# Kernel optimization log

Hardware: AMD Instinct MI355X
Metric: run time of the kernel (lower is better)

Reference implementation:

```python
import jax, jax.numpy as jnp
import numpy as np

D_MODEL = 256
EXPAND = 2
MAX_STEPS = 6
DILATIONS = (1, 2, 4)
EPS = 1e-6


def setup_inputs() -> dict:
    key = jax.random.key(0)
    ks = jax.random.split(key, 12)
    B, C, H, W = 8, D_MODEL, 64, 64
    d, dh = D_MODEL, D_MODEL * EXPAND
    init_logit = float(np.log(0.1 / (0.25 - 0.1 + 1e-08)))
    s = 1.0 / np.sqrt(d)
    return {
        "u": jax.random.normal(ks[0], (B, C, H, W), jnp.float32),
        "forcing": jax.random.normal(ks[1], (B, C, H, W), jnp.float32),
        "diff_logits": jnp.full((3, d), init_logit, jnp.float32),
        "w1": jax.random.uniform(ks[2], (d, dh), jnp.float32, -s, s),
        "b1": jax.random.uniform(ks[3], (dh,), jnp.float32, -s, s),
        "w2": jax.random.uniform(ks[4], (dh, d), jnp.float32, -1.0 / np.sqrt(dh), 1.0 / np.sqrt(dh)),
        "b2": jax.random.uniform(ks[5], (d,), jnp.float32, -1.0 / np.sqrt(dh), 1.0 / np.sqrt(dh)),
        "wf": jax.random.uniform(ks[6], (d, d), jnp.float32, -s, s),
        "bf": jax.random.uniform(ks[7], (d,), jnp.float32, -s, s),
        "wi": jax.random.uniform(ks[8], (d, d), jnp.float32, -s, s),
        "bi": jax.random.uniform(ks[9], (d,), jnp.float32, -s, s),
        "wc": jax.random.uniform(ks[10], (d, d), jnp.float32, -s, s),
        "bc": jax.random.uniform(ks[11], (d,), jnp.float32, -s, s),
        "norm_scale": jnp.ones((d,), jnp.float32),
        "log_dt": jnp.asarray(np.log(0.1), jnp.float32),
        "alpha_mem": jnp.asarray(0.1, jnp.float32),
        "alpha_force": jnp.asarray(0.1, jnp.float32),
    }


def _laplacian(u, diff_logits):
    # multi-dilation 5-point reflect-padded stencil, per-channel coeffs
    out = jnp.zeros_like(u)
    for i, d in enumerate(DILATIONS):
        coeff = 0.25 * jax.nn.sigmoid(diff_logits[i])  # (C,)
        p = jnp.pad(u, ((0, 0), (0, 0), (d, d), (d, d)), mode="reflect")
        lap = (p[:, :, d:-d, 2 * d:] + p[:, :, d:-d, :-2 * d]
               + p[:, :, 2 * d:, d:-d] + p[:, :, :-2 * d, d:-d] - 4.0 * u)
        out = out + coeff[None, :, None, None] * lap
    return out


def reference(u, forcing, diff_logits, w1, b1, w2, b2, wf, bf, wi, bi, wc, bc,
              norm_scale, log_dt, alpha_mem, alpha_force):
    B, C, H, W = u.shape
    dt = jnp.clip(jnp.exp(log_dt), 0.01, 0.3)
    h = jnp.zeros((B, C), u.dtype)
    inv_sqrt_c = 1.0 / float(np.sqrt(C))
    for t in range(MAX_STEPS):
        diff = _laplacian(u, diff_logits)
        # per-cell reaction MLP on channel axis (exact GELU, matching torch)
        hdn = jax.nn.gelu(jnp.einsum("bchw,ce->behw", u, w1) + b1[None, :, None, None],
                          approximate=False)
        react = jnp.einsum("behw,ec->bchw", hdn, w2) + b2[None, :, None, None]
        # gated global memory on pooled features
        pooled = u.mean(axis=(2, 3))  # (B, C)
        f = jax.nn.sigmoid(pooled @ wf + bf)
        i_ = jax.nn.sigmoid(pooled @ wi + bi)
        c = jnp.tanh(pooled @ wc + bc)
        h = h * f + i_ * c
        du = diff + react + alpha_mem * h[:, :, None, None] + alpha_force * forcing
        u = u + dt * du
        if (t + 1) % 2 == 0:
            # RMSNorm over channel dim
            rms = jnp.sqrt(jnp.sum(u * u, axis=1, keepdims=True)) * inv_sqrt_c
            u = u / (rms + EPS) * norm_scale[None, :, None, None]
    return u
```

## Files before the change

### kernel.cpp

```cpp
#include <hip/hip_runtime.h>
#include <math.h>

constexpr int NB = 8, NC = 256, NE = 512, NH = 64, NW = 64, NHW = NH * NW;
constexpr int STEPS = 6;

typedef short bfrag8 __attribute__((ext_vector_type(8)));
typedef float f32x4 __attribute__((ext_vector_type(4)));

__device__ __forceinline__ float sigm_(float x) { return 1.f / (1.f + expf(-x)); }
__device__ __forceinline__ float gelu_(float x) {
    const float t2 = fmaf(0.0713548162f * x, x * x, 1.5957691216f * x);
    return x / (1.f + __expf(-t2));
}
__device__ __forceinline__ ushort f2bf(float f) {
    unsigned u = __builtin_bit_cast(unsigned, f);
    unsigned r = (u + 0x7fffu + ((u >> 16) & 1u)) >> 16;
    return (ushort)r;
}
__device__ __forceinline__ float bf2f(ushort us) {
    return __builtin_bit_cast(float, (unsigned)us << 16);
}
__device__ __forceinline__ void gload16(const void* g, void* l) {
    __builtin_amdgcn_global_load_lds((const __attribute__((address_space(1))) void*)g,
                                     (__attribute__((address_space(3))) void*)l, 16, 0, 0);
}

__global__ void wt_kernel(const float* __restrict__ w1, const float* __restrict__ w2,
                          const float* __restrict__ dlog,
                          const float* __restrict__ wf, const float* __restrict__ wi,
                          const float* __restrict__ wc,
                          ushort* __restrict__ w1t, ushort* __restrict__ w2t,
                          float* __restrict__ dcoef, ushort* __restrict__ wgb) {
    const int bid = blockIdx.x, tid = threadIdx.x;
    if (bid < NE) {
        w1t[bid * NC + tid] = f2bf(w1[(size_t)tid * NE + bid]);
    } else if (bid < NE + NC) {
        const int c = bid - NE;
        for (int e = tid; e < NE; e += 256)
            w2t[c * NE + e] = f2bf(w2[(size_t)e * NC + c]);
    } else if (bid == NE + NC) {
#pragma unroll
        for (int i = 0; i < 3; ++i)
            dcoef[i * NC + tid] = 0.25f * sigm_(dlog[i * NC + tid]);
    } else {
        const int k = bid - (NE + NC + 1);
        wgb[(0 * NC + k) * NC + tid] = f2bf(wf[(size_t)k * NC + tid]);
        wgb[(1 * NC + k) * NC + tid] = f2bf(wi[(size_t)k * NC + tid]);
        wgb[(2 * NC + k) * NC + tid] = f2bf(wc[(size_t)k * NC + tid]);
    }
}

__global__ void fconv_kernel(const float* __restrict__ fin, ushort* __restrict__ fout) {
    const size_t i8 = ((size_t)blockIdx.x * 256 + threadIdx.x) * 8;
    const float4 a = *reinterpret_cast<const float4*>(fin + i8);
    const float4 b = *reinterpret_cast<const float4*>(fin + i8 + 4);
    uint4 o;
    o.x = (unsigned)f2bf(a.x) | ((unsigned)f2bf(a.y) << 16);
    o.y = (unsigned)f2bf(a.z) | ((unsigned)f2bf(a.w) << 16);
    o.z = (unsigned)f2bf(b.x) | ((unsigned)f2bf(b.y) << 16);
    o.w = (unsigned)f2bf(b.z) | ((unsigned)f2bf(b.w) << 16);
    *reinterpret_cast<uint4*>(fout + i8) = o;
}

__global__ __launch_bounds__(256) void rs0_kernel(const float* __restrict__ u,
                                                  float* __restrict__ rowsums) {
    const int b = blockIdx.x >> 6, y = blockIdx.x & 63;
    const int c = threadIdx.x;
    const float* rp = u + ((size_t)b * NC + c) * NHW + (size_t)y * NW;
    float s = 0.f;
#pragma unroll
    for (int i = 0; i < 16; ++i) {
        const float4 v = *reinterpret_cast<const float4*>(rp + i * 4);
        s += (v.x + v.y) + (v.z + v.w);
    }
    rowsums[((size_t)b * 64 + y) * NC + c] = s;
}

__global__ __launch_bounds__(768) void gates_kernel(
    const float* __restrict__ rowsums, const ushort* __restrict__ wgb,
    const float* __restrict__ bfv, const float* __restrict__ biv,
    const float* __restrict__ bcv,
    float* __restrict__ h, const int first) {
    const int b = blockIdx.x;
    const int tid = threadIdx.x;
    const int g = tid >> 8, c = tid & 255;
    __shared__ float sp[256];
    __shared__ float psum[3][256];
    __shared__ float gf[256], gi[256];
    const int y0 = (g == 0) ? 0 : (g == 1) ? 21 : 42;
    const int y1 = (g == 0) ? 21 : (g == 1) ? 42 : 64;
    const float* rs = rowsums + (size_t)b * 64 * NC + c;
    float s = 0.f;
    for (int y = y0; y < y1; ++y) s += rs[y * NC];
    psum[g][c] = s;
    __syncthreads();
    if (g == 0) sp[c] = (psum[0][c] + psum[1][c] + psum[2][c]) * (1.f / 4096.f);
    __syncthreads();
    const ushort* W16 = wgb + (size_t)g * NC * NC;
    const float* Bv = (g == 0) ? bfv : (g == 1) ? biv : bcv;
    float aA = 0.f, aB = 0.f, aC = 0.f, aD = 0.f;
#pragma unroll 4
    for (int k = 0; k < 256; k += 4) {
        aA = fmaf(sp[k],     bf2f(W16[(k)     * NC + c]), aA);
        aB = fmaf(sp[k + 1], bf2f(W16[(k + 1) * NC + c]), aB);
        aC = fmaf(sp[k + 2], bf2f(W16[(k + 2) * NC + c]), aC);
        aD = fmaf(sp[k + 3], bf2f(W16[(k + 3) * NC + c]), aD);
    }
    const float a = ((aA + aB) + (aC + aD)) + Bv[c];
    if (g == 0) gf[c] = sigm_(a);
    else if (g == 1) gi[c] = sigm_(a);
    __syncthreads();
    if (g == 2) {
        const float cc = tanhf(a);
        const float hold = first ? 0.f : h[b * NC + c];
        h[b * NC + c] = hold * gf[c] + gi[c] * cc;
    }
}

__global__ __launch_bounds__(512, 4) void step_kernel(
    const ushort* __restrict__ w1t, const ushort* __restrict__ w2t,
    const float* __restrict__ b1, const float* __restrict__ b2,
    const float* __restrict__ uin, const ushort* __restrict__ forc,
    const float* __restrict__ dcoef, const float* __restrict__ hbuf,
    const float* __restrict__ nsc, const float* __restrict__ p_logdt,
    const float* __restrict__ p_am, const float* __restrict__ p_af,
    const int do_norm, float* __restrict__ uout, float* __restrict__ rowsums) {
    __shared__ __align__(16) char pool[75776];
    ushort* Xs  = (ushort*)pool;
    ushort* WAu = (ushort*)(pool + 32768);
    ushort* WBu = (ushort*)(pool + 49152);
    ushort* Hsu = (ushort*)(pool + 65536);

    const int tid = threadIdx.x;
    const int wv = tid >> 6, lane = tid & 63;
    const int r16 = lane & 15, kg = lane >> 4;
    const int work = (blockIdx.x & 7) * 64 + (blockIdx.x >> 3);
    const int b = work >> 6, y = work & 63;

    const float* ub = uin + (size_t)b * NC * NHW;
    const float* uyb = ub + (size_t)y * NW;

#pragma unroll
    for (int i = 0; i < 2; ++i) {
        const int idx = i * 512 + tid, row = idx >> 5, s = idx & 31;
        gload16(w1t + (size_t)row * NC + ((s ^ (row & 7)) << 3), WAu + idx * 8);
    }
#pragma unroll
    for (int tt = 0; tt < 2; ++tt) {
        const int id = tt * 512 + tid;
        const int pg_ = id & 15, cg_ = id >> 4;
        const int px0 = pg_ * 4, c0 = cg_ * 4;
        const float4 r0 = *(const float4*)(uyb + (size_t)(c0 + 0) * NHW + px0);
        const float4 r1 = *(const float4*)(uyb + (size_t)(c0 + 1) * NHW + px0);
        const float4 r2 = *(const float4*)(uyb + (size_t)(c0 + 2) * NHW + px0);
        const float4 r3 = *(const float4*)(uyb + (size_t)(c0 + 3) * NHW + px0);
        const int slot = c0 >> 3, sub = c0 & 7;
        const float a0[4] = {r0.x, r0.y, r0.z, r0.w};
        const float a1[4] = {r1.x, r1.y, r1.z, r1.w};
        const float a2[4] = {r2.x, r2.y, r2.z, r2.w};
        const float a3[4] = {r3.x, r3.y, r3.z, r3.w};
#pragma unroll
        for (int i2 = 0; i2 < 4; ++i2) {
            const int px = px0 + i2;
            ushort4 xv;
            xv.x = f2bf(a0[i2]);
            xv.y = f2bf(a1[i2]);
            xv.z = f2bf(a2[i2]);
            xv.w = f2bf(a3[i2]);
            *(ushort4*)(Xs + px * 256 + ((slot ^ (px & 7)) << 3) + sub) = xv;
        }
    }

    f32x4 acc2[2][4];
#pragma unroll
    for (int ct = 0; ct < 2; ++ct)
#pragma unroll
        for (int p = 0; p < 4; ++p) acc2[ct][p] = (f32x4){0.f, 0.f, 0.f, 0.f};

    const int eh = wv >> 2, pq = wv & 3;
    __syncthreads();

    bfrag8 xf[8];
    {
        const int rB = pq * 16 + r16;
#pragma unroll
        for (int kk = 0; kk < 8; ++kk) {
            const int g = kk * 4 + kg;
            xf[kk] = *(const bfrag8*)(Xs + rB * 256 + ((g ^ (rB & 7)) << 3));
        }
    }

    for (int ec = 0; ec < 16; ++ec) {
#pragma unroll
        for (int i = 0; i < 2; ++i) {
            const int idx = i * 512 + tid, row = idx >> 2, s = idx & 3;
            const int sc = (s ^ ((row >> 1) & 3)) << 3;
            gload16(w2t + (size_t)row * NE + ec * 32 + sc, WBu + idx * 8);
        }
        f32x4 acc1 = (f32x4){0.f, 0.f, 0.f, 0.f};
        const int rA = eh * 16 + r16;
#pragma unroll
        for (int kk = 0; kk < 8; ++kk) {
            const int g = kk * 4 + kg;
            const bfrag8 a = *(const bfrag8*)(WAu + rA * 256 + ((g ^ (rA & 7)) << 3));
            acc1 = __builtin_amdgcn_mfma_f32_16x16x32_bf16(a, xf[kk], acc1, 0, 0, 0);
        }
        ushort* Hc = Hsu + (ec & 1) * 2560;
        {
            const int el = eh * 16 + kg * 4;
            const float4 b1v = *(const float4*)(b1 + ec * 32 + el);
            ushort4 hv;
            hv.x = f2bf(gelu_(acc1[0] + b1v.x));
            hv.y = f2bf(gelu_(acc1[1] + b1v.y));
            hv.z = f2bf(gelu_(acc1[2] + b1v.z));
            hv.w = f2bf(gelu_(acc1[3] + b1v.w));
            *(ushort4*)(Hc + (pq * 16 + r16) * 40 + el) = hv;
        }
        __syncthreads();
        if (ec < 15) {
#pragma unroll
            for (int i = 0; i < 2; ++i) {
                const int idx = i * 512 + tid, row = idx >> 5, s = idx & 31;
                gload16(w1t + (size_t)((ec + 1) * 32 + row) * NC + ((s ^ (row & 7)) << 3),
                        WAu + idx * 8);
            }
        }
#pragma unroll
        for (int ct = 0; ct < 2; ++ct) {
            const int rowA = wv * 32 + ct * 16 + r16;
            const bfrag8 a2 = *(const bfrag8*)(WBu + rowA * 32 + ((kg ^ ((rowA >> 1) & 3)) << 3));
#pragma unroll
            for (int p = 0; p < 4; ++p) {
                const bfrag8 bf2 = *(const bfrag8*)(Hc + (p * 16 + r16) * 40 + kg * 8);
                acc2[ct][p] = __builtin_amdgcn_mfma_f32_16x16x32_bf16(a2, bf2, acc2[ct][p], 0, 0, 0);
            }
        }
        __syncthreads();
    }

    float* trh = (float*)pool;
    float* su  = (float*)(pool + 35328);
    const int eg2 = tid >> 4, pg = tid & 15, x0p = pg * 4;
    const float dt = fminf(fmaxf(expf(p_logdt[0]), 0.01f), 0.3f);
    const float am = p_am[0], afc = p_af[0];
    const ushort* frow = forc + (size_t)b * NC * NHW + (size_t)y * NW;

    float unew[2][4][4];

#pragma unroll
    for (int h2 = 0; h2 < 2; ++h2) {
        __syncthreads();
        if ((wv >> 2) == h2) {
#pragma unroll
            for (int ct = 0; ct < 2; ++ct)
#pragma unroll
                for (int p = 0; p < 4; ++p)
#pragma unroll
                    for (int j = 0; j < 4; ++j)
                        trh[((wv & 3) * 32 + ct * 16 + kg * 4 + j) * 69 + p * 16 + r16] =
                            acc2[ct][p][j];
        }
#pragma unroll
        for (int i = 0; i < 4; ++i) {
            const int idx = i * 512 + tid;
            const int r = idx >> 4, q = (idx & 15) * 4;
            *(float4*)&su[r * 69 + q] =
                *(const float4*)(ub + (size_t)(h2 * 128 + r) * NHW + (size_t)y * NW + q);
        }
        __syncthreads();
#pragma unroll
        for (int jc = 0; jc < 4; ++jc) {
            const int crel = eg2 * 4 + jc;
            const int c = h2 * 128 + crel;
            const float co0 = dcoef[c];
            const float co1 = dcoef[NC + c];
            const float co2 = dcoef[2 * NC + c];
            const float hterm = am * hbuf[b * NC + c];
            const float b2v = b2[c];
            const float* up = ub + (size_t)c * NHW;

            float ym[6][4];
            const int dy[6] = {-1, 1, -2, 2, -4, 4};
#pragma unroll
            for (int n = 0; n < 6; ++n) {
                int ry = y + dy[n];
                ry = ry < 0 ? -ry : (ry > 63 ? 126 - ry : ry);
                const float4 t = *reinterpret_cast<const float4*>(up + (size_t)ry * NW + x0p);
                ym[n][0] = t.x; ym[n][1] = t.y; ym[n][2] = t.z; ym[n][3] = t.w;
            }
            const uint2 fr = *reinterpret_cast<const uint2*>(frow + (size_t)c * NHW + x0p);
            float fv[4];
            fv[0] = bf2f((ushort)(fr.x & 0xffff));
            fv[1] = bf2f((ushort)(fr.x >> 16));
            fv[2] = bf2f((ushort)(fr.y & 0xffff));
            fv[3] = bf2f((ushort)(fr.y >> 16));
            const f32x4 rv = *reinterpret_cast<const f32x4*>(&trh[crel * 69 + x0p]);
#pragma unroll
            for (int ip = 0; ip < 4; ++ip) {
                const int x = x0p + ip;
                const float uc = su[crel * 69 + x];
                int xm, xp2;
                float dsum = 0.f, lap;
                xm = x - 1; xm = xm < 0 ? -xm : xm;
                xp2 = x + 1; xp2 = xp2 > 63 ? 126 - xp2 : xp2;
                lap = su[crel * 69 + xm] + su[crel * 69 + xp2] + ym[0][ip] + ym[1][ip] - 4.f * uc;
                dsum = fmaf(co0, lap, dsum);
                xm = x - 2; xm = xm < 0 ? -xm : xm;
                xp2 = x + 2; xp2 = xp2 > 63 ? 126 - xp2 : xp2;
                lap = su[crel * 69 + xm] + su[crel * 69 + xp2] + ym[2][ip] + ym[3][ip] - 4.f * uc;
                dsum = fmaf(co1, lap, dsum);
                xm = x - 4; xm = xm < 0 ? -xm : xm;
                xp2 = x + 4; xp2 = xp2 > 63 ? 126 - xp2 : xp2;
                lap = su[crel * 69 + xm] + su[crel * 69 + xp2] + ym[4][ip] + ym[5][ip] - 4.f * uc;
                dsum = fmaf(co2, lap, dsum);

                const float du_ = dsum + rv[ip] + b2v + hterm + afc * fv[ip];
                unew[h2][jc][ip] = uc + dt * du_;
            }
        }
    }
    __syncthreads();

    float* redc   = (float*)(pool + 35328);
    float* inv64p = (float*)(pool + 70656);
    if (do_norm) {
        float ps[4] = {0.f, 0.f, 0.f, 0.f};
#pragma unroll
        for (int h2 = 0; h2 < 2; ++h2)
#pragma unroll
            for (int jc = 0; jc < 4; ++jc)
#pragma unroll
                for (int ip = 0; ip < 4; ++ip)
                    ps[ip] = fmaf(unew[h2][jc][ip], unew[h2][jc][ip], ps[ip]);
        *reinterpret_cast<f32x4*>(&redc[eg2 * 69 + x0p]) = (f32x4){ps[0], ps[1], ps[2], ps[3]};
        __syncthreads();
        if (tid < 64) {
            float s = 0.f;
#pragma unroll
            for (int g = 0; g < 32; ++g) s += redc[g * 69 + tid];
            inv64p[tid] = 1.f / (sqrtf(s) * 0.0625f + 1e-6f);
        }
    }
    __syncthreads();

    float* sums = (float*)(pool + 35328);
    float persum[2][4];
    float* uob = uout + (size_t)b * NC * NHW + (size_t)y * NW;
#pragma unroll
    for (int h2 = 0; h2 < 2; ++h2) {
#pragma unroll
        for (int jc = 0; jc < 4; ++jc) {
            const int c = h2 * 128 + eg2 * 4 + jc;
            const float ns = do_norm ? nsc[c] : 1.f;
            float vv[4];
#pragma unroll
            for (int ip = 0; ip < 4; ++ip) {
                float v = unew[h2][jc][ip];
                if (do_norm) v *= inv64p[x0p + ip] * ns;
                vv[ip] = v;
            }
            persum[h2][jc] = (vv[0] + vv[1]) + (vv[2] + vv[3]);
            float4 o; o.x = vv[0]; o.y = vv[1]; o.z = vv[2]; o.w = vv[3];
            *reinterpret_cast<float4*>(uob + (size_t)c * NHW + x0p) = o;
            sums[c * 17 + pg] = persum[h2][jc];
        }
    }
    __syncthreads();
    if (tid < 256) {
        float s = 0.f;
#pragma unroll
        for (int g = 0; g < 16; ++g) s += sums[tid * 17 + g];
        rowsums[((size_t)b * 64 + y) * NC + tid] = s;
    }
}

extern "C" void kernel_launch(void* const* d_in, const int* in_sizes, int n_in,
                              void* d_out, int out_size, void* d_ws, size_t ws_size,
                              hipStream_t stream) {
    (void)in_sizes; (void)n_in; (void)out_size; (void)ws_size;
    const float* u0      = (const float*)d_in[0];
    const float* forcing = (const float*)d_in[1];
    const float* dlog    = (const float*)d_in[2];
    const float* w1      = (const float*)d_in[3];
    const float* b1      = (const float*)d_in[4];
    const float* w2      = (const float*)d_in[5];
    const float* b2      = (const float*)d_in[6];
    const float* wf      = (const float*)d_in[7];
    const float* bfv     = (const float*)d_in[8];
    const float* wi      = (const float*)d_in[9];
    const float* biv     = (const float*)d_in[10];
    const float* wc      = (const float*)d_in[11];
    const float* bcv     = (const float*)d_in[12];
    const float* nsc     = (const float*)d_in[13];
    const float* p_logdt = (const float*)d_in[14];
    const float* p_am    = (const float*)d_in[15];
    const float* p_af    = (const float*)d_in[16];

    float* uout = (float*)d_out;

    char* w = (char*)d_ws;
    float*  uA     = (float*)w;   w += (size_t)NB * NC * NHW * 4;
    ushort* forc   = (ushort*)w;  w += (size_t)NB * NC * NHW * 2;
    ushort* w1t    = (ushort*)w;  w += (size_t)NE * NC * 2;
    ushort* w2t    = (ushort*)w;  w += (size_t)NC * NE * 2;
    ushort* wgb    = (ushort*)w;  w += (size_t)3 * NC * NC * 2;
    float* rowsums = (float*)w;   w += (size_t)NB * NH * NC * 4;
    float* hbuf    = (float*)w;   w += (size_t)NB * NC * 4;
    float* dcoef   = (float*)w;   w += (size_t)3 * NC * 4;

    wt_kernel<<<NE + NC + 1 + NC, 256, 0, stream>>>(w1, w2, dlog, wf, wi, wc,
                                                    w1t, w2t, dcoef, wgb);
    fconv_kernel<<<4096, 256, 0, stream>>>(forcing, forc);
    rs0_kernel<<<NB * NH, 256, 0, stream>>>(u0, rowsums);

    const float* src = u0;
    for (int t = 0; t < STEPS; ++t) {
        float* dst = (t & 1) ? uout : uA;
        gates_kernel<<<NB, 768, 0, stream>>>(rowsums, wgb, bfv, biv, bcv, hbuf, t == 0);
        step_kernel<<<NB * NH, 512, 0, stream>>>(w1t, w2t, b1, b2, src, forc, dcoef,
                                                 hbuf, nsc, p_logdt, p_am, p_af,
                                                 ((t + 1) % 2) == 0, dst, rowsums);
        src = dst;
    }
}
```

Measured before the change: 575.1 us.

## Fuse gated memory computation into step kernel and pad stencil rows

Removes the separate gates kernel launch per step: every step block redundantly reduces the pooled row sums, computes the f/i/c gates from transposed bf16 weights, and updates h, with row sums and h ping-ponged between buffers to avoid races. The horizontal stencil now reads from a reflect-padded shared row using vector loads instead of per-element index clamping. This trades six small serial launches for redundant gate GEMV work in all 512 blocks plus extra shared memory and syncs, which may lower occupancy.

```diff
diff --git a/kernel.cpp b/kernel.cpp
--- a/kernel.cpp
+++ b/kernel.cpp
@@ -30,7 +30,7 @@
                           const float* __restrict__ wf, const float* __restrict__ wi,
                           const float* __restrict__ wc,
                           ushort* __restrict__ w1t, ushort* __restrict__ w2t,
-                          float* __restrict__ dcoef, ushort* __restrict__ wgb) {
+                          float* __restrict__ dcoef, ushort* __restrict__ wgt) {
     const int bid = blockIdx.x, tid = threadIdx.x;
     if (bid < NE) {
         w1t[bid * NC + tid] = f2bf(w1[(size_t)tid * NE + bid]);
@@ -43,10 +43,10 @@
         for (int i = 0; i < 3; ++i)
             dcoef[i * NC + tid] = 0.25f * sigm_(dlog[i * NC + tid]);
     } else {
-        const int k = bid - (NE + NC + 1);
-        wgb[(0 * NC + k) * NC + tid] = f2bf(wf[(size_t)k * NC + tid]);
-        wgb[(1 * NC + k) * NC + tid] = f2bf(wi[(size_t)k * NC + tid]);
-        wgb[(2 * NC + k) * NC + tid] = f2bf(wc[(size_t)k * NC + tid]);
+        const int j = bid - (NE + NC + 1);
+        const int g = j >> 8, c = j & 255, k = tid;
+        const float* src = (g == 0) ? wf : (g == 1) ? wi : wc;
+        wgt[(((size_t)g * NC + c) << 8) + k] = f2bf(src[(size_t)k * NC + c]);
     }
 }
 
@@ -76,60 +76,26 @@
     rowsums[((size_t)b * 64 + y) * NC + c] = s;
 }
 
-__global__ __launch_bounds__(768) void gates_kernel(
-    const float* __restrict__ rowsums, const ushort* __restrict__ wgb,
-    const float* __restrict__ bfv, const float* __restrict__ biv,
-    const float* __restrict__ bcv,
-    float* __restrict__ h, const int first) {
-    const int b = blockIdx.x;
-    const int tid = threadIdx.x;
-    const int g = tid >> 8, c = tid & 255;
-    __shared__ float sp[256];
-    __shared__ float psum[3][256];
-    __shared__ float gf[256], gi[256];
-    const int y0 = (g == 0) ? 0 : (g == 1) ? 21 : 42;
-    const int y1 = (g == 0) ? 21 : (g == 1) ? 42 : 64;
-    const float* rs = rowsums + (size_t)b * 64 * NC + c;
-    float s = 0.f;
-    for (int y = y0; y < y1; ++y) s += rs[y * NC];
-    psum[g][c] = s;
-    __syncthreads();
-    if (g == 0) sp[c] = (psum[0][c] + psum[1][c] + psum[2][c]) * (1.f / 4096.f);
-    __syncthreads();
-    const ushort* W16 = wgb + (size_t)g * NC * NC;
-    const float* Bv = (g == 0) ? bfv : (g == 1) ? biv : bcv;
-    float aA = 0.f, aB = 0.f, aC = 0.f, aD = 0.f;
-#pragma unroll 4
-    for (int k = 0; k < 256; k += 4) {
-        aA = fmaf(sp[k],     bf2f(W16[(k)     * NC + c]), aA);
-        aB = fmaf(sp[k + 1], bf2f(W16[(k + 1) * NC + c]), aB);
-        aC = fmaf(sp[k + 2], bf2f(W16[(k + 2) * NC + c]), aC);
-        aD = fmaf(sp[k + 3], bf2f(W16[(k + 3) * NC + c]), aD);
-    }
-    const float a = ((aA + aB) + (aC + aD)) + Bv[c];
-    if (g == 0) gf[c] = sigm_(a);
-    else if (g == 1) gi[c] = sigm_(a);
-    __syncthreads();
-    if (g == 2) {
-        const float cc = tanhf(a);
-        const float hold = first ? 0.f : h[b * NC + c];
-        h[b * NC + c] = hold * gf[c] + gi[c] * cc;
-    }
-}
-
 __global__ __launch_bounds__(512, 4) void step_kernel(
     const ushort* __restrict__ w1t, const ushort* __restrict__ w2t,
     const float* __restrict__ b1, const float* __restrict__ b2,
     const float* __restrict__ uin, const ushort* __restrict__ forc,
-    const float* __restrict__ dcoef, const float* __restrict__ hbuf,
-    const float* __restrict__ nsc, const float* __restrict__ p_logdt,
-    const float* __restrict__ p_am, const float* __restrict__ p_af,
-    const int do_norm, float* __restrict__ uout, float* __restrict__ rowsums) {
-    __shared__ __align__(16) char pool[75776];
+    const float* __restrict__ dcoef, const ushort* __restrict__ wgt,
+    const float* __restrict__ bfv, const float* __restrict__ biv,
+    const float* __restrict__ bcv, const float* __restrict__ hprev,
+    float* __restrict__ hnext, const float* __restrict__ rs_in,
+    float* __restrict__ rs_out, const float* __restrict__ nsc,
+    const float* __restrict__ p_logdt, const float* __restrict__ p_am,
+    const float* __restrict__ p_af, const int do_norm, const int first,
+    float* __restrict__ uout) {
+    __shared__ __align__(16) char pool[79872];
     ushort* Xs  = (ushort*)pool;
     ushort* WAu = (ushort*)(pool + 32768);
     ushort* WBu = (ushort*)(pool + 49152);
     ushort* Hsu = (ushort*)(pool + 65536);
+    float* gsp  = (float*)(pool + 75776);
+    float* gex  = (float*)(pool + 76800);
+    float* hseg = (float*)(pool + 77824);
 
     const int tid = threadIdx.x;
     const int wv = tid >> 6, lane = tid & 63;
@@ -137,6 +103,7 @@
     const int work = (blockIdx.x & 7) * 64 + (blockIdx.x >> 3);
     const int b = work >> 6, y = work & 63;
 
+    const float am = p_am[0];
     const float* ub = uin + (size_t)b * NC * NHW;
     const float* uyb = ub + (size_t)y * NW;
 
@@ -170,6 +137,14 @@
             *(ushort4*)(Xs + px * 256 + ((slot ^ (px & 7)) << 3) + sub) = xv;
         }
     }
+    {
+        const int gc = tid & 255, half = tid >> 8;
+        const float* rs = rs_in + ((size_t)b * 64 + half * 32) * NC + gc;
+        float s = 0.f;
+#pragma unroll 8
+        for (int yy = 0; yy < 32; ++yy) s += rs[yy * NC];
+        (half ? gex : gsp)[gc] = s;
+    }
 
     f32x4 acc2[2][4];
 #pragma unroll
@@ -188,6 +163,55 @@
             const int g = kk * 4 + kg;
             xf[kk] = *(const bfrag8*)(Xs + rB * 256 + ((g ^ (rB & 7)) << 3));
         }
+    }
+    if (tid < 256) gsp[tid] = (gsp[tid] + gex[tid]) * (1.f / 4096.f);
+    __syncthreads();
+
+    float gfv = 0.f, ccv = 0.f;
+    {
+        const int gc = tid & 255, g1 = tid >> 8;
+        const ushort* wrow = wgt + (((size_t)g1 * NC + gc) << 8);
+        float a0 = 0.f, a1 = 0.f;
+#pragma unroll 4
+        for (int k8 = 0; k8 < 256; k8 += 8) {
+            const uint4 wv4 = *(const uint4*)(wrow + k8);
+            a0 = fmaf(gsp[k8 + 0], bf2f((ushort)(wv4.x & 0xffff)), a0);
+            a1 = fmaf(gsp[k8 + 1], bf2f((ushort)(wv4.x >> 16)), a1);
+            a0 = fmaf(gsp[k8 + 2], bf2f((ushort)(wv4.y & 0xffff)), a0);
+            a1 = fmaf(gsp[k8 + 3], bf2f((ushort)(wv4.y >> 16)), a1);
+            a0 = fmaf(gsp[k8 + 4], bf2f((ushort)(wv4.z & 0xffff)), a0);
+            a1 = fmaf(gsp[k8 + 5], bf2f((ushort)(wv4.z >> 16)), a1);
+            a0 = fmaf(gsp[k8 + 6], bf2f((ushort)(wv4.w & 0xffff)), a0);
+            a1 = fmaf(gsp[k8 + 7], bf2f((ushort)(wv4.w >> 16)), a1);
+        }
+        const float av = (a0 + a1) + (g1 == 0 ? bfv[gc] : biv[gc]);
+        if (g1 == 0) gfv = sigm_(av);
+        else gex[gc] = sigm_(av);
+        if (tid < 256) {
+            const ushort* wrow2 = wgt + (((size_t)2 * NC + gc) << 8);
+            float c0 = 0.f, c1 = 0.f;
+#pragma unroll 4
+            for (int k8 = 0; k8 < 256; k8 += 8) {
+                const uint4 wv4 = *(const uint4*)(wrow2 + k8);
+                c0 = fmaf(gsp[k8 + 0], bf2f((ushort)(wv4.x & 0xffff)), c0);
+                c1 = fmaf(gsp[k8 + 1], bf2f((ushort)(wv4.x >> 16)), c1);
+                c0 = fmaf(gsp[k8 + 2], bf2f((ushort)(wv4.y & 0xffff)), c0);
+                c1 = fmaf(gsp[k8 + 3], bf2f((ushort)(wv4.y >> 16)), c1);
+                c0 = fmaf(gsp[k8 + 4], bf2f((ushort)(wv4.z & 0xffff)), c0);
+                c1 = fmaf(gsp[k8 + 5], bf2f((ushort)(wv4.z >> 16)), c1);
+                c0 = fmaf(gsp[k8 + 6], bf2f((ushort)(wv4.w & 0xffff)), c0);
+                c1 = fmaf(gsp[k8 + 7], bf2f((ushort)(wv4.w >> 16)), c1);
+            }
+            ccv = tanhf((c0 + c1) + bcv[gc]);
+        }
+    }
+    __syncthreads();
+    if (tid < 256) {
+        const int gc = tid;
+        const float hp = first ? 0.f : hprev[b * NC + gc];
+        const float h = hp * gfv + gex[gc] * ccv;
+        hseg[gc] = am * h;
+        if (y == 0) hnext[b * NC + gc] = h;
     }
 
     for (int ec = 0; ec < 16; ++ec) {
@@ -242,7 +266,7 @@
     float* su  = (float*)(pool + 35328);
     const int eg2 = tid >> 4, pg = tid & 15, x0p = pg * 4;
     const float dt = fminf(fmaxf(expf(p_logdt[0]), 0.01f), 0.3f);
-    const float am = p_am[0], afc = p_af[0];
+    const float afc = p_af[0];
     const ushort* frow = forc + (size_t)b * NC * NHW + (size_t)y * NW;
 
     float unew[2][4][4];
@@ -264,8 +288,15 @@
         for (int i = 0; i < 4; ++i) {
             const int idx = i * 512 + tid;
             const int r = idx >> 4, q = (idx & 15) * 4;
-            *(float4*)&su[r * 69 + q] =
+            *(float4*)&su[r * 72 + 4 + q] =
                 *(const float4*)(ub + (size_t)(h2 * 128 + r) * NHW + (size_t)y * NW + q);
+        }
+        if (tid < 256) {
+            const int r = tid >> 1, side = tid & 1;
+            const float* gp = ub + (size_t)(h2 * 128 + r) * NHW + (size_t)y * NW;
+            float* sr = &su[r * 72];
+            if (side == 0) { sr[0] = gp[4]; sr[1] = gp[3]; sr[2] = gp[2]; sr[3] = gp[1]; }
+            else { sr[68] = gp[62]; sr[69] = gp[61]; sr[70] = gp[60]; sr[71] = gp[59]; }
         }
         __syncthreads();
 #pragma unroll
@@ -275,7 +306,7 @@
             const float co0 = dcoef[c];
             const float co1 = dcoef[NC + c];
             const float co2 = dcoef[2 * NC + c];
-            const float hterm = am * hbuf[b * NC + c];
+            const float hterm = hseg[c];
             const float b2v = b2[c];
             const float* up = ub + (size_t)c * NHW;
 
@@ -295,23 +326,21 @@
             fv[2] = bf2f((ushort)(fr.y & 0xffff));
             fv[3] = bf2f((ushort)(fr.y >> 16));
             const f32x4 rv = *reinterpret_cast<const f32x4*>(&trh[crel * 69 + x0p]);
+            const f32x4 wm = *reinterpret_cast<const f32x4*>(&su[crel * 72 + pg * 4]);
+            const f32x4 wc4 = *reinterpret_cast<const f32x4*>(&su[crel * 72 + 4 + pg * 4]);
+            const f32x4 wp = *reinterpret_cast<const f32x4*>(&su[crel * 72 + 8 + pg * 4]);
+            const float w[12] = {wm[0], wm[1], wm[2], wm[3],
+                                 wc4[0], wc4[1], wc4[2], wc4[3],
+                                 wp[0], wp[1], wp[2], wp[3]};
 #pragma unroll
             for (int ip = 0; ip < 4; ++ip) {
-                const int x = x0p + ip;
-                const float uc = su[crel * 69 + x];
-                int xm, xp2;
-                float dsum = 0.f, lap;
-                xm = x - 1; xm = xm < 0 ? -xm : xm;
-                xp2 = x + 1; xp2 = xp2 > 63 ? 126 - xp2 : xp2;
-                lap = su[crel * 69 + xm] + su[crel * 69 + xp2] + ym[0][ip] + ym[1][ip] - 4.f * uc;
-                dsum = fmaf(co0, lap, dsum);
-                xm = x - 2; xm = xm < 0 ? -xm : xm;
-                xp2 = x + 2; xp2 = xp2 > 63 ? 126 - xp2 : xp2;
-                lap = su[crel * 69 + xm] + su[crel * 69 + xp2] + ym[2][ip] + ym[3][ip] - 4.f * uc;
+                const float uc = w[4 + ip];
+                float dsum;
+                float lap = (w[3 + ip] + w[5 + ip]) + (ym[0][ip] + ym[1][ip]) - 4.f * uc;
+                dsum = co0 * lap;
+                lap = (w[2 + ip] + w[6 + ip]) + (ym[2][ip] + ym[3][ip]) - 4.f * uc;
                 dsum = fmaf(co1, lap, dsum);
-                xm = x - 4; xm = xm < 0 ? -xm : xm;
-                xp2 = x + 4; xp2 = xp2 > 63 ? 126 - xp2 : xp2;
-                lap = su[crel * 69 + xm] + su[crel * 69 + xp2] + ym[4][ip] + ym[5][ip] - 4.f * uc;
+                lap = (w[ip] + w[8 + ip]) + (ym[4][ip] + ym[5][ip]) - 4.f * uc;
                 dsum = fmaf(co2, lap, dsum);
 
                 const float du_ = dsum + rv[ip] + b2v + hterm + afc * fv[ip];
@@ -322,7 +351,7 @@
     __syncthreads();
 
     float* redc   = (float*)(pool + 35328);
-    float* inv64p = (float*)(pool + 70656);
+    float* inv64p = (float*)(pool + 73728);
     if (do_norm) {
         float ps[4] = {0.f, 0.f, 0.f, 0.f};
 #pragma unroll
@@ -344,7 +373,6 @@
     __syncthreads();
 
     float* sums = (float*)(pool + 35328);
-    float persum[2][4];
     float* uob = uout + (size_t)b * NC * NHW + (size_t)y * NW;
 #pragma unroll
     for (int h2 = 0; h2 < 2; ++h2) {
@@ -359,10 +387,9 @@
                 if (do_norm) v *= inv64p[x0p + ip] * ns;
                 vv[ip] = v;
             }
-            persum[h2][jc] = (vv[0] + vv[1]) + (vv[2] + vv[3]);
             float4 o; o.x = vv[0]; o.y = vv[1]; o.z = vv[2]; o.w = vv[3];
             *reinterpret_cast<float4*>(uob + (size_t)c * NHW + x0p) = o;
-            sums[c * 17 + pg] = persum[h2][jc];
+            sums[c * 17 + pg] = (vv[0] + vv[1]) + (vv[2] + vv[3]);
         }
     }
     __syncthreads();
@@ -370,7 +397,7 @@
         float s = 0.f;
 #pragma unroll
         for (int g = 0; g < 16; ++g) s += sums[tid * 17 + g];
-        rowsums[((size_t)b * 64 + y) * NC + tid] = s;
+        rs_out[((size_t)b * 64 + y) * NC + tid] = s;
     }
 }
 
@@ -403,23 +430,31 @@
     ushort* forc   = (ushort*)w;  w += (size_t)NB * NC * NHW * 2;
     ushort* w1t    = (ushort*)w;  w += (size_t)NE * NC * 2;
     ushort* w2t    = (ushort*)w;  w += (size_t)NC * NE * 2;
-    ushort* wgb    = (ushort*)w;  w += (size_t)3 * NC * NC * 2;
-    float* rowsums = (float*)w;   w += (size_t)NB * NH * NC * 4;
-    float* hbuf    = (float*)w;   w += (size_t)NB * NC * 4;
+    ushort* wgt    = (ushort*)w;  w += (size_t)3 * NC * NC * 2;
+    float* rsA     = (float*)w;   w += (size_t)NB * NH * NC * 4;
+    float* rsB     = (float*)w;   w += (size_t)NB * NH * NC * 4;
+    float* hA      = (float*)w;   w += (size_t)NB * NC * 4;
+    float* hB      = (float*)w;   w += (size_t)NB * NC * 4;
     float* dcoef   = (float*)w;   w += (size_t)3 * NC * 4;
 
-    wt_kernel<<<NE + NC + 1 + NC, 256, 0, stream>>>(w1, w2, dlog, wf, wi, wc,
-                                                    w1t, w2t, dcoef, wgb);
+    wt_kernel<<<NE + NC + 1 + 3 * NC, 256, 0, stream>>>(w1, w2, dlog, wf, wi, wc,
+                                                        w1t, w2t, dcoef, wgt);
     fconv_kernel<<<4096, 256, 0, stream>>>(forcing, forc);
-    rs0_kernel<<<NB * NH, 256, 0, stream>>>(u0, rowsums);
+    rs0_kernel<<<NB * NH, 256, 0, stream>>>(u0, rsA);
 
     const float* src = u0;
+    const float* rs_in = rsA;
+    float* rs_out = rsB;
+    float* hbufs[2] = {hA, hB};
     for (int t = 0; t < STEPS; ++t) {
         float* dst = (t & 1) ? uout : uA;
-        gates_kernel<<<NB, 768, 0, stream>>>(rowsums, wgb, bfv, biv, bcv, hbuf, t == 0);
+        const float* hp = hbufs[t & 1];
+        float* hn = hbufs[(t + 1) & 1];
         step_kernel<<<NB * NH, 512, 0, stream>>>(w1t, w2t, b1, b2, src, forc, dcoef,
-                                                 hbuf, nsc, p_logdt, p_am, p_af,
-                                                 ((t + 1) % 2) == 0, dst, rowsums);
+                                                 wgt, bfv, biv, bcv, hp, hn,
+                                                 rs_in, rs_out, nsc, p_logdt, p_am, p_af,
+                                                 ((t + 1) % 2) == 0, t == 0, dst);
         src = dst;
-    }
-}
+        const float* tmp = rs_in; rs_in = rs_out; rs_out = (float*)tmp;
+    }
+}
```

Result: no change. 585.8 us (+1.9%).
